# Kernel tuning notes

Hardware: AMD Instinct MI355X
Metric: run time of the kernel (lower is better)

Reference implementation:

```python
import jax, jax.numpy as jnp
import numpy as np

N, D_IN, D_H, N_HEADS, N_CLS = 8192, 384, 64, 4, 6
LN_EPS = 1e-5


def setup_inputs() -> dict:
    key = jax.random.key(0)
    ks = jax.random.split(key, 8)
    x = jax.random.normal(ks[0], (N, D_IN), dtype=jnp.float32)
    proj_w = jax.random.normal(ks[1], (D_IN, D_H), dtype=jnp.float32) / np.sqrt(D_IN)
    proj_b = jnp.zeros((D_H,), jnp.float32)
    head_w = jax.random.normal(ks[2], (N_HEADS, D_H, D_H), dtype=jnp.float32) / np.sqrt(D_H)
    head_b = jnp.zeros((N_HEADS, D_H), jnp.float32)
    attn_w = jnp.ones((N_HEADS,), jnp.float32)  # nn.Parameter(torch.ones(num_heads))
    gamma = jnp.ones((D_H,), jnp.float32)
    beta = jnp.zeros((D_H,), jnp.float32)
    fc_w = jax.random.normal(ks[3], (D_H, N_CLS), dtype=jnp.float32) / np.sqrt(D_H)
    fc_b = jnp.zeros((N_CLS,), jnp.float32)
    return {"x": x, "proj_w": proj_w, "proj_b": proj_b, "head_w": head_w,
            "head_b": head_b, "attn_w": attn_w, "gamma": gamma, "beta": beta,
            "fc_w": fc_w, "fc_b": fc_b}


def _safe_cdist_sq_to_dist(sq):
    # Euclidean distance with zero (sub)gradient at zero distance, matching torch.cdist.
    pos = sq > 0
    return jnp.where(pos, jnp.sqrt(jnp.where(pos, sq, 1.0)), 0.0)


def reference(x, proj_w, proj_b, head_w, head_b, attn_w, gamma, beta, fc_w, fc_b):
    h = jax.nn.relu(x @ proj_w + proj_b)                      # [N, D_H]
    hp = jnp.einsum('nd,hde->hne', h, head_w) + head_b[:, None, :]  # [H, N, D_H]
    sumsq = jnp.sum(hp * hp, axis=-1)                          # [H, N]
    sq = sumsq[:, :, None] + sumsq[:, None, :] - 2.0 * jnp.einsum('hnd,hmd->hnm', hp, hp)
    dist = _safe_cdist_sq_to_dist(jnp.maximum(sq, 0.0))        # [H, N, N]
    scores = jax.nn.softmax(-dist, axis=-1)                    # [H, N, N]
    h_head = jnp.einsum('hnm,hmd->hnd', scores, hp)            # [H, N, D_H]
    aw = jax.nn.softmax(attn_w, axis=0)                        # [H]
    combined = jnp.einsum('h,hnd->nd', aw, h_head)             # [N, D_H]
    mu = jnp.mean(combined, axis=-1, keepdims=True)
    var = jnp.mean((combined - mu) ** 2, axis=-1, keepdims=True)
    normed = (combined - mu) * jax.lax.rsqrt(var + LN_EPS) * gamma + beta
    return normed @ fc_w + fc_b                                # [N, N_CLS]
```

## Files before the change

### kernel.cpp

```cpp
#include <hip/hip_runtime.h>

#define N_TOK 8192
#define D_IN 384
#define D_H 64
#define NHEADS 4
#define NSPLIT 4
#define N_CLS 6
#define LN_EPS 1e-5f

typedef __attribute__((ext_vector_type(8))) short short8;
typedef __attribute__((ext_vector_type(4))) float f32x4;

#define L2E2 2.08136898100560774f

__device__ __forceinline__ unsigned short f2bf(float f) {
    unsigned int u = __float_as_uint(f);
    u += 0x7FFFu + ((u >> 16) & 1u);
    return (unsigned short)(u >> 16);
}
__device__ __forceinline__ float bf2f(unsigned short s) {
    return __uint_as_float(((unsigned int)s) << 16);
}

__device__ __forceinline__ int kperm(int k) {
    return (k & 32) + 2 * (k & 15) + ((k >> 4) & 1);
}

__device__ __forceinline__ void gload_lds16(const void* g, void* l) {
    __builtin_amdgcn_global_load_lds(
        (const __attribute__((address_space(1))) unsigned int*)g,
        (__attribute__((address_space(3))) unsigned int*)l, 16, 0, 0);
}

__global__ __launch_bounds__(512) void stage1_kernel(
    const float* __restrict__ x, const float* __restrict__ proj_w,
    const float* __restrict__ proj_b, const float* __restrict__ head_w,
    const float* __restrict__ head_b,
    unsigned short* __restrict__ hp, unsigned short* __restrict__ Vf,
    float* __restrict__ ssq2)
{
    const int lane = threadIdx.x & 63;
    const int wv   = threadIdx.x >> 6;
    const int rb0  = blockIdx.x * 32;

    __shared__ float h_sh[32][68];
    __shared__ __align__(16) unsigned short vt[NHEADS][4][64][8];

    {
        float acc[4];
        float b = proj_b[lane];
        #pragma unroll
        for (int r = 0; r < 4; ++r) acc[r] = b;
        const float* x0 = x + (size_t)(rb0 + wv * 4) * D_IN;
        #pragma unroll 2
        for (int k4 = 0; k4 < D_IN / 4; ++k4) {
            float w0 = proj_w[(k4 * 4 + 0) * 64 + lane];
            float w1 = proj_w[(k4 * 4 + 1) * 64 + lane];
            float w2 = proj_w[(k4 * 4 + 2) * 64 + lane];
            float w3 = proj_w[(k4 * 4 + 3) * 64 + lane];
            #pragma unroll
            for (int r = 0; r < 4; ++r) {
                float4 xv = *(const float4*)(x0 + r * D_IN + k4 * 4);
                acc[r] = fmaf(xv.x, w0, acc[r]);
                acc[r] = fmaf(xv.y, w1, acc[r]);
                acc[r] = fmaf(xv.z, w2, acc[r]);
                acc[r] = fmaf(xv.w, w3, acc[r]);
            }
        }
        #pragma unroll
        for (int r = 0; r < 4; ++r)
            h_sh[wv * 4 + r][lane] = fmaxf(acc[r], 0.f);
    }
    __syncthreads();

    const int head = wv >> 1;
    const int half = wv & 1;
    float a[16];
    {
        float b = head_b[head * 64 + lane];
        #pragma unroll
        for (int r = 0; r < 16; ++r) a[r] = b;
    }
    const float* wb = head_w + head * 64 * 64;
    #pragma unroll 2
    for (int e4 = 0; e4 < 16; ++e4) {
        float w0 = wb[(e4 * 4 + 0) * 64 + lane];
        float w1 = wb[(e4 * 4 + 1) * 64 + lane];
        float w2 = wb[(e4 * 4 + 2) * 64 + lane];
        float w3 = wb[(e4 * 4 + 3) * 64 + lane];
        #pragma unroll
        for (int r = 0; r < 16; ++r) {
            float4 hv = *(const float4*)&h_sh[half * 16 + r][e4 * 4];
            a[r] = fmaf(hv.x, w0, a[r]);
            a[r] = fmaf(hv.y, w1, a[r]);
            a[r] = fmaf(hv.z, w2, a[r]);
            a[r] = fmaf(hv.w, w3, a[r]);
        }
    }

    #pragma unroll
    for (int r = 0; r < 16; ++r) {
        int kl  = half * 16 + r;
        int row = rb0 + kl;
        unsigned short hb = f2bf(a[r]);
        float hf = bf2f(hb);
        hp[((size_t)head * N_TOK + row) * 64 + lane] = hb;
        int p = kperm(row & 63);
        vt[head][(p >> 3) & 3][lane][p & 7] = hb;
        float s = hf * hf;
        #pragma unroll
        for (int off = 32; off > 0; off >>= 1) s += __shfl_xor(s, off);
        if (lane == 0) ssq2[head * N_TOK + row] = s * L2E2;
    }
    __syncthreads();

    const int kgbase = (rb0 & 32) ? 4 : 0;
    #pragma unroll
    for (int i = 0; i < 2; ++i) {
        int c  = threadIdx.x + 512 * i;
        int hc = c >> 8, rem = c & 255;
        int kg = rem >> 6, d = rem & 63;
        short8 v = *(const short8*)&vt[hc][kg][d][0];
        *(short8*)&Vf[(((size_t)hc * (N_TOK / 8) + (rb0 >> 6) * 8 + kgbase + kg) * 64
                       + d) * 8] = v;
    }
}

__global__ __launch_bounds__(256, 4) void flash_kernel(
    const unsigned short* __restrict__ hp, const unsigned short* __restrict__ Vf,
    const float* __restrict__ ssq2, unsigned short* __restrict__ Og,
    float* __restrict__ Lg)
{
    const int head  = blockIdx.x & 3;
    const int split = blockIdx.x >> 2;
    const int q0    = blockIdx.y * 128;
    const int w     = threadIdx.x >> 6;
    const int lane  = threadIdx.x & 63;
    const int col   = lane & 15;
    const int quad  = lane >> 4;
    const int tid   = threadIdx.x;

    __shared__ __align__(16) unsigned short Psh[4][2][16][64];
    __shared__ __align__(16) unsigned short Kst[2][4096];
    __shared__ __align__(16) unsigned short Vst[2][4096];

    const unsigned short* hpH = hp + head * (N_TOK * 64);
    const unsigned short* VfH = Vf + head * (N_TOK * 64);
    const float* ssqH = ssq2 + head * N_TOK;

    const int rb = q0 + w * 32;
    const bool diag_lo = ((rb >> 5) & 1) == 0;

    short8 aQ[2][2];
    float ssqn2[2][4];
    #pragma unroll
    for (int s = 0; s < 2; ++s) {
        const unsigned short* qrow = hpH + (rb + s * 16 + col) * 64;
        aQ[s][0] = *(const short8*)(qrow + quad * 8);
        aQ[s][1] = *(const short8*)(qrow + 32 + quad * 8);
        #pragma unroll
        for (int r = 0; r < 4; ++r)
            ssqn2[s][r] = ssqH[rb + s * 16 + quad * 4 + r];
    }

    const f32x4 zero4 = {0.f, 0.f, 0.f, 0.f};
    f32x4 accO[2][4] = {{zero4, zero4, zero4, zero4}, {zero4, zero4, zero4, zero4}};
    f32x4 accL[2] = {zero4, zero4};
    const short8 ones = {16256,16256,16256,16256,16256,16256,16256,16256};
    const float NEG2L2 = -2.0f * L2E2;

    const int koff0 = (((tid & ~7) | ((tid & 7) ^ ((tid >> 3) & 7))) << 4);
    const int karow = col * 128 + ((quad ^ (col & 7)) << 4);
    const int va    = (quad * 64 + col) << 4;
    const int wcb   = quad * 512 + ((((col >> 2) ^ ((quad & 1) << 2)) << 4))
                      + ((col & 3) << 2);

    const int kt0   = split * 32;
    const int ktend = kt0 + 32;

    {
        const char* kg = (const char*)(hpH + kt0 * 4096);
        const char* vg = (const char*)(VfH + kt0 * 4096);
        gload_lds16(kg + koff0,        (char*)&Kst[0][0] + tid * 16);
        gload_lds16(kg + koff0 + 4096, (char*)&Kst[0][0] + tid * 16 + 4096);
        gload_lds16(vg + tid * 16,        (char*)&Vst[0][0] + tid * 16);
        gload_lds16(vg + tid * 16 + 4096, (char*)&Vst[0][0] + tid * 16 + 4096);
    }
    float smc[4];
    #pragma unroll
    for (int nt = 0; nt < 4; ++nt) smc[nt] = ssqH[kt0 * 64 + nt * 16 + col];
    __syncthreads();

    #pragma unroll 1
    for (int kt = kt0; kt < ktend; ++kt) {
        const int p = (kt - kt0) & 1;
        const char* Kb = (const char*)&Kst[p][0];
        const char* Vb = (const char*)&Vst[p][0];
        const bool has_next = (kt + 1 < ktend);

        float smn[4];
        if (has_next) {
            const char* kgn = (const char*)(hpH + (kt + 1) * 4096);
            const char* vgn = (const char*)(VfH + (kt + 1) * 4096);
            char* Kn = (char*)&Kst[p ^ 1][0];
            char* Vn = (char*)&Vst[p ^ 1][0];
            gload_lds16(kgn + koff0,        Kn + tid * 16);
            gload_lds16(kgn + koff0 + 4096, Kn + tid * 16 + 4096);
            gload_lds16(vgn + tid * 16,        Vn + tid * 16);
            gload_lds16(vgn + tid * 16 + 4096, Vn + tid * 16 + 4096);
            #pragma unroll
            for (int nt = 0; nt < 4; ++nt)
                smn[nt] = ssqH[(kt + 1) * 64 + nt * 16 + col];
        }

        f32x4 aSA[2][2] = {{zero4, zero4}, {zero4, zero4}};
        {
            short8 k0 = *(const short8*)(Kb + karow);
            short8 k1 = *(const short8*)(Kb + (karow ^ 64));
            short8 k2 = *(const short8*)(Kb + 2048 + karow);
            short8 k3 = *(const short8*)(Kb + 2048 + (karow ^ 64));
            aSA[0][0] = __builtin_amdgcn_mfma_f32_16x16x32_bf16(aQ[0][0], k0, aSA[0][0], 0, 0, 0);
            aSA[0][0] = __builtin_amdgcn_mfma_f32_16x16x32_bf16(aQ[0][1], k1, aSA[0][0], 0, 0, 0);
            aSA[1][0] = __builtin_amdgcn_mfma_f32_16x16x32_bf16(aQ[1][0], k0, aSA[1][0], 0, 0, 0);
            aSA[1][0] = __builtin_amdgcn_mfma_f32_16x16x32_bf16(aQ[1][1], k1, aSA[1][0], 0, 0, 0);
            aSA[0][1] = __builtin_amdgcn_mfma_f32_16x16x32_bf16(aQ[0][0], k2, aSA[0][1], 0, 0, 0);
            aSA[0][1] = __builtin_amdgcn_mfma_f32_16x16x32_bf16(aQ[0][1], k3, aSA[0][1], 0, 0, 0);
            aSA[1][1] = __builtin_amdgcn_mfma_f32_16x16x32_bf16(aQ[1][0], k2, aSA[1][1], 0, 0, 0);
            aSA[1][1] = __builtin_amdgcn_mfma_f32_16x16x32_bf16(aQ[1][1], k3, aSA[1][1], 0, 0, 0);
        }

        #pragma unroll
        for (int s = 0; s < 2; ++s) {
            char* pB = (char*)&Psh[w][s][0][0];
            float pf0[4], pf1[4];
            #pragma unroll
            for (int r = 0; r < 4; ++r) {
                float sq0 = fmaf(aSA[s][0][r], NEG2L2, ssqn2[s][r] + smc[0]);
                pf0[r] = __builtin_amdgcn_exp2f(-__builtin_amdgcn_sqrtf(fmaxf(sq0, 0.f)));
                float sq1 = fmaf(aSA[s][1][r], NEG2L2, ssqn2[s][r] + smc[1]);
                pf1[r] = __builtin_amdgcn_exp2f(-__builtin_amdgcn_sqrtf(fmaxf(sq1, 0.f)));
            }
            #pragma unroll
            for (int r = 0; r < 4; ++r) {
                unsigned int d0 = __builtin_amdgcn_perm(__float_as_uint(pf1[r]),
                                                        __float_as_uint(pf0[r]), 0x07060302u);
                *(unsigned int*)(pB + ((wcb ^ (r << 4)) + r * 128)) = d0;
            }
        }
        if (diag_lo && kt == (rb >> 6) && lane < 16) {
            #pragma unroll
            for (int s = 0; s < 2; ++s) {
                int t = ((rb + s * 16) >> 4) & 3;
                int sc2 = 4 * lane + 2 * (t & 1);
                int ad = lane * 128 + (((lane >> 2) ^ (lane & 7)) << 4) + (sc2 & 15);
                *(unsigned short*)((char*)&Psh[w][s][0][0] + ad) = 0x3F80;
            }
        }

        f32x4 aSB[2][2] = {{zero4, zero4}, {zero4, zero4}};
        {
            short8 k0 = *(const short8*)(Kb + 4096 + karow);
            short8 k1 = *(const short8*)(Kb + 4096 + (karow ^ 64));
            short8 k2 = *(const short8*)(Kb + 6144 + karow);
            short8 k3 = *(const short8*)(Kb + 6144 + (karow ^ 64));
            aSB[0][0] = __builtin_amdgcn_mfma_f32_16x16x32_bf16(aQ[0][0], k0, aSB[0][0], 0, 0, 0);
            aSB[0][0] = __builtin_amdgcn_mfma_f32_16x16x32_bf16(aQ[0][1], k1, aSB[0][0], 0, 0, 0);
            aSB[1][0] = __builtin_amdgcn_mfma_f32_16x16x32_bf16(aQ[1][0], k0, aSB[1][0], 0, 0, 0);
            aSB[1][0] = __builtin_amdgcn_mfma_f32_16x16x32_bf16(aQ[1][1], k1, aSB[1][0], 0, 0, 0);
            aSB[0][1] = __builtin_amdgcn_mfma_f32_16x16x32_bf16(aQ[0][0], k2, aSB[0][1], 0, 0, 0);
            aSB[0][1] = __builtin_amdgcn_mfma_f32_16x16x32_bf16(aQ[0][1], k3, aSB[0][1], 0, 0, 0);
            aSB[1][1] = __builtin_amdgcn_mfma_f32_16x16x32_bf16(aQ[1][0], k2, aSB[1][1], 0, 0, 0);
            aSB[1][1] = __builtin_amdgcn_mfma_f32_16x16x32_bf16(aQ[1][1], k3, aSB[1][1], 0, 0, 0);
        }

        #pragma unroll
        for (int s = 0; s < 2; ++s) {
            char* pB = (char*)&Psh[w][s][0][0];
            float pf2[4], pf3[4];
            #pragma unroll
            for (int r = 0; r < 4; ++r) {
                float sq2 = fmaf(aSB[s][0][r], NEG2L2, ssqn2[s][r] + smc[2]);
                pf2[r] = __builtin_amdgcn_exp2f(-__builtin_amdgcn_sqrtf(fmaxf(sq2, 0.f)));
                float sq3 = fmaf(aSB[s][1][r], NEG2L2, ssqn2[s][r] + smc[3]);
                pf3[r] = __builtin_amdgcn_exp2f(-__builtin_amdgcn_sqrtf(fmaxf(sq3, 0.f)));
            }
            #pragma unroll
            for (int r = 0; r < 4; ++r) {
                unsigned int d1 = __builtin_amdgcn_perm(__float_as_uint(pf3[r]),
                                                        __float_as_uint(pf2[r]), 0x07060302u);
                *(unsigned int*)(pB + (((wcb ^ (r << 4)) + r * 128) ^ 64)) = d1;
            }
        }
        if (!diag_lo && kt == (rb >> 6) && lane < 16) {
            #pragma unroll
            for (int s = 0; s < 2; ++s) {
                int t = ((rb + s * 16) >> 4) & 3;
                int sc2 = 4 * lane + 2 * (t & 1);
                int ad = (lane * 128 + (((lane >> 2) ^ (lane & 7)) << 4) + (sc2 & 15)) ^ 64;
                *(unsigned short*)((char*)&Psh[w][s][0][0] + ad) = 0x3F80;
            }
        }

        {
            const char* p0 = (const char*)&Psh[w][0][0][0];
            const char* p1 = (const char*)&Psh[w][1][0][0];
            short8 aP0 = *(const short8*)(p0 + karow);
            short8 aP1 = *(const short8*)(p1 + karow);
            short8 bV[4];
            #pragma unroll
            for (int dt = 0; dt < 4; ++dt)
                bV[dt] = *(const short8*)(Vb + va + dt * 256);
            accL[0] = __builtin_amdgcn_mfma_f32_16x16x32_bf16(aP0, ones, accL[0], 0, 0, 0);
            accL[1] = __builtin_amdgcn_mfma_f32_16x16x32_bf16(aP1, ones, accL[1], 0, 0, 0);
            #pragma unroll
            for (int dt = 0; dt < 4; ++dt) {
                accO[0][dt] = __builtin_amdgcn_mfma_f32_16x16x32_bf16(aP0, bV[dt], accO[0][dt], 0, 0, 0);
                accO[1][dt] = __builtin_amdgcn_mfma_f32_16x16x32_bf16(aP1, bV[dt], accO[1][dt], 0, 0, 0);
            }
            short8 aP0b = *(const short8*)(p0 + (karow ^ 64));
            short8 aP1b = *(const short8*)(p1 + (karow ^ 64));
            #pragma unroll
            for (int dt = 0; dt < 4; ++dt)
                bV[dt] = *(const short8*)(Vb + va + dt * 256 + 4096);
            accL[0] = __builtin_amdgcn_mfma_f32_16x16x32_bf16(aP0b, ones, accL[0], 0, 0, 0);
            accL[1] = __builtin_amdgcn_mfma_f32_16x16x32_bf16(aP1b, ones, accL[1], 0, 0, 0);
            #pragma unroll
            for (int dt = 0; dt < 4; ++dt) {
                accO[0][dt] = __builtin_amdgcn_mfma_f32_16x16x32_bf16(aP0b, bV[dt], accO[0][dt], 0, 0, 0);
                accO[1][dt] = __builtin_amdgcn_mfma_f32_16x16x32_bf16(aP1b, bV[dt], accO[1][dt], 0, 0, 0);
            }
        }

        __syncthreads();
        if (has_next) {
            smc[0] = smn[0]; smc[1] = smn[1]; smc[2] = smn[2]; smc[3] = smn[3];
        }
    }

    unsigned short* og = Og + (size_t)(split * NHEADS + head) * N_TOK * 64;
    float* lg = Lg + (size_t)(split * NHEADS + head) * N_TOK;
    #pragma unroll
    for (int s = 0; s < 2; ++s)
        #pragma unroll
        for (int r = 0; r < 4; ++r) {
            int row = rb + s * 16 + quad * 4 + r;
            #pragma unroll
            for (int dt = 0; dt < 4; ++dt)
                og[row * 64 + dt * 16 + col] = f2bf(accO[s][dt][r]);
            if (col == 0) lg[row] = accL[s][r];
        }
}

__global__ __launch_bounds__(256) void combine_kernel(
    const unsigned short* __restrict__ Og, const float* __restrict__ Lg,
    const float* __restrict__ attn_w, const float* __restrict__ gamma,
    const float* __restrict__ beta, const float* __restrict__ fc_w,
    const float* __restrict__ fc_b, float* __restrict__ out)
{
    const int lane = threadIdx.x & 63;
    const int ty   = threadIdx.x >> 6;
    const int row  = blockIdx.x * 4 + ty;

    float a0 = attn_w[0], a1 = attn_w[1], a2 = attn_w[2], a3 = attn_w[3];
    float m = fmaxf(fmaxf(a0, a1), fmaxf(a2, a3));
    float e0 = __expf(a0 - m), e1 = __expf(a1 - m), e2 = __expf(a2 - m), e3 = __expf(a3 - m);
    float inv = 1.f / (e0 + e1 + e2 + e3);
    float aw[4] = {e0 * inv, e1 * inv, e2 * inv, e3 * inv};

    float c = 0.f;
    #pragma unroll
    for (int hh = 0; hh < NHEADS; ++hh) {
        float l = 0.f, o = 0.f;
        #pragma unroll
        for (int s = 0; s < NSPLIT; ++s) {
            l += Lg[(s * NHEADS + hh) * N_TOK + row];
            o += bf2f(Og[(size_t)((s * NHEADS + hh) * N_TOK + row) * 64 + lane]);
        }
        c += aw[hh] * o * __builtin_amdgcn_rcpf(l);
    }

    float s = c;
    #pragma unroll
    for (int off = 32; off > 0; off >>= 1) s += __shfl_xor(s, off);
    float mu = s * (1.f / 64.f);
    float d = c - mu;
    float v = d * d;
    #pragma unroll
    for (int off = 32; off > 0; off >>= 1) v += __shfl_xor(v, off);
    float normed = d * rsqrtf(v * (1.f / 64.f) + LN_EPS) * gamma[lane] + beta[lane];

    float lg[N_CLS];
    #pragma unroll
    for (int cc = 0; cc < N_CLS; ++cc) {
        float p = normed * fc_w[lane * N_CLS + cc];
        #pragma unroll
        for (int off = 32; off > 0; off >>= 1) p += __shfl_xor(p, off);
        lg[cc] = p;
    }
    if (lane == 0) {
        #pragma unroll
        for (int cc = 0; cc < N_CLS; ++cc)
            out[row * N_CLS + cc] = lg[cc] + fc_b[cc];
    }
}

extern "C" void kernel_launch(void* const* d_in, const int* in_sizes, int n_in,
                              void* d_out, int out_size, void* d_ws, size_t ws_size,
                              hipStream_t stream)
{
    const float* x      = (const float*)d_in[0];
    const float* proj_w = (const float*)d_in[1];
    const float* proj_b = (const float*)d_in[2];
    const float* head_w = (const float*)d_in[3];
    const float* head_b = (const float*)d_in[4];
    const float* attn_w = (const float*)d_in[5];
    const float* gamma  = (const float*)d_in[6];
    const float* beta   = (const float*)d_in[7];
    const float* fc_w   = (const float*)d_in[8];
    const float* fc_b   = (const float*)d_in[9];
    float* out = (float*)d_out;

    char* ws = (char*)d_ws;
    unsigned short* hp = (unsigned short*)(ws);
    unsigned short* Vf = (unsigned short*)(ws + (4u << 20));
    float* ssq2 = (float*)(ws + (8u << 20));
    unsigned short* Og = (unsigned short*)(ws + (8u << 20) + (128u << 10));
    float* Lg   = (float*)(ws + (24u << 20) + (128u << 10));

    stage1_kernel<<<N_TOK / 32, 512, 0, stream>>>(x, proj_w, proj_b, head_w, head_b,
                                                  hp, Vf, ssq2);
    dim3 g2(NHEADS * NSPLIT, N_TOK / 128);
    flash_kernel<<<g2, 256, 0, stream>>>(hp, Vf, ssq2, Og, Lg);
    combine_kernel<<<N_TOK / 4, 256, 0, stream>>>(Og, Lg, attn_w, gamma, beta,
                                                  fc_w, fc_b, out);
}
```

Baseline: 234.0 us.

## Process query sub-tiles sequentially per warp with single P staging buffer

Restructures the inner flash loop so each warp handles its two 16-row query sub-tiles one after another. Each pass runs the full QK^T, the exp/sqrt scoring and the PV accumulation before moving on, instead of splitting the key tile into two halves across both sub-tiles. This halves the per-warp P staging buffer in shared memory and simplifies the diagonal fixup. In exchange, K and V fragments are reloaded from LDS once per sub-tile, and there is less independent MFMA work in flight to hide latency.

Result: slower. 419.0 us (+79.1%).

```diff
diff --git a/kernel.cpp b/kernel.cpp
--- a/kernel.cpp
+++ b/kernel.cpp
@@ -140,7 +140,7 @@
     const int quad  = lane >> 4;
     const int tid   = threadIdx.x;
 
-    __shared__ __align__(16) unsigned short Psh[4][2][16][64];
+    __shared__ __align__(16) unsigned short Psh[4][16][64];
     __shared__ __align__(16) unsigned short Kst[2][4096];
     __shared__ __align__(16) unsigned short Vst[2][4096];
 
@@ -149,7 +149,6 @@
     const float* ssqH = ssq2 + head * N_TOK;
 
     const int rb = q0 + w * 32;
-    const bool diag_lo = ((rb >> 5) & 1) == 0;
 
     short8 aQ[2][2];
     float ssqn2[2][4];
@@ -213,121 +212,78 @@
                 smn[nt] = ssqH[(kt + 1) * 64 + nt * 16 + col];
         }
 
-        f32x4 aSA[2][2] = {{zero4, zero4}, {zero4, zero4}};
-        {
-            short8 k0 = *(const short8*)(Kb + karow);
-            short8 k1 = *(const short8*)(Kb + (karow ^ 64));
-            short8 k2 = *(const short8*)(Kb + 2048 + karow);
-            short8 k3 = *(const short8*)(Kb + 2048 + (karow ^ 64));
-            aSA[0][0] = __builtin_amdgcn_mfma_f32_16x16x32_bf16(aQ[0][0], k0, aSA[0][0], 0, 0, 0);
-            aSA[0][0] = __builtin_amdgcn_mfma_f32_16x16x32_bf16(aQ[0][1], k1, aSA[0][0], 0, 0, 0);
-            aSA[1][0] = __builtin_amdgcn_mfma_f32_16x16x32_bf16(aQ[1][0], k0, aSA[1][0], 0, 0, 0);
-            aSA[1][0] = __builtin_amdgcn_mfma_f32_16x16x32_bf16(aQ[1][1], k1, aSA[1][0], 0, 0, 0);
-            aSA[0][1] = __builtin_amdgcn_mfma_f32_16x16x32_bf16(aQ[0][0], k2, aSA[0][1], 0, 0, 0);
-            aSA[0][1] = __builtin_amdgcn_mfma_f32_16x16x32_bf16(aQ[0][1], k3, aSA[0][1], 0, 0, 0);
-            aSA[1][1] = __builtin_amdgcn_mfma_f32_16x16x32_bf16(aQ[1][0], k2, aSA[1][1], 0, 0, 0);
-            aSA[1][1] = __builtin_amdgcn_mfma_f32_16x16x32_bf16(aQ[1][1], k3, aSA[1][1], 0, 0, 0);
-        }
+        char* pB = (char*)&Psh[w][0][0];
 
         #pragma unroll
         for (int s = 0; s < 2; ++s) {
-            char* pB = (char*)&Psh[w][s][0][0];
-            float pf0[4], pf1[4];
-            #pragma unroll
-            for (int r = 0; r < 4; ++r) {
-                float sq0 = fmaf(aSA[s][0][r], NEG2L2, ssqn2[s][r] + smc[0]);
-                pf0[r] = __builtin_amdgcn_exp2f(-__builtin_amdgcn_sqrtf(fmaxf(sq0, 0.f)));
-                float sq1 = fmaf(aSA[s][1][r], NEG2L2, ssqn2[s][r] + smc[1]);
-                pf1[r] = __builtin_amdgcn_exp2f(-__builtin_amdgcn_sqrtf(fmaxf(sq1, 0.f)));
-            }
-            #pragma unroll
-            for (int r = 0; r < 4; ++r) {
-                unsigned int d0 = __builtin_amdgcn_perm(__float_as_uint(pf1[r]),
-                                                        __float_as_uint(pf0[r]), 0x07060302u);
-                *(unsigned int*)(pB + ((wcb ^ (r << 4)) + r * 128)) = d0;
-            }
-        }
-        if (diag_lo && kt == (rb >> 6) && lane < 16) {
-            #pragma unroll
-            for (int s = 0; s < 2; ++s) {
+            f32x4 aS[4] = {zero4, zero4, zero4, zero4};
+            {
+                short8 k0 = *(const short8*)(Kb + karow);
+                short8 k1 = *(const short8*)(Kb + (karow ^ 64));
+                short8 k2 = *(const short8*)(Kb + 2048 + karow);
+                short8 k3 = *(const short8*)(Kb + 2048 + (karow ^ 64));
+                aS[0] = __builtin_amdgcn_mfma_f32_16x16x32_bf16(aQ[s][0], k0, aS[0], 0, 0, 0);
+                aS[0] = __builtin_amdgcn_mfma_f32_16x16x32_bf16(aQ[s][1], k1, aS[0], 0, 0, 0);
+                aS[1] = __builtin_amdgcn_mfma_f32_16x16x32_bf16(aQ[s][0], k2, aS[1], 0, 0, 0);
+                aS[1] = __builtin_amdgcn_mfma_f32_16x16x32_bf16(aQ[s][1], k3, aS[1], 0, 0, 0);
+                k0 = *(const short8*)(Kb + 4096 + karow);
+                k1 = *(const short8*)(Kb + 4096 + (karow ^ 64));
+                k2 = *(const short8*)(Kb + 6144 + karow);
+                k3 = *(const short8*)(Kb + 6144 + (karow ^ 64));
+                aS[2] = __builtin_amdgcn_mfma_f32_16x16x32_bf16(aQ[s][0], k0, aS[2], 0, 0, 0);
+                aS[2] = __builtin_amdgcn_mfma_f32_16x16x32_bf16(aQ[s][1], k1, aS[2], 0, 0, 0);
+                aS[3] = __builtin_amdgcn_mfma_f32_16x16x32_bf16(aQ[s][0], k2, aS[3], 0, 0, 0);
+                aS[3] = __builtin_amdgcn_mfma_f32_16x16x32_bf16(aQ[s][1], k3, aS[3], 0, 0, 0);
+            }
+
+            {
+                float pf[4][4];
+                #pragma unroll
+                for (int nt = 0; nt < 4; ++nt)
+                    #pragma unroll
+                    for (int r = 0; r < 4; ++r) {
+                        float sq = fmaf(aS[nt][r], NEG2L2, ssqn2[s][r] + smc[nt]);
+                        pf[nt][r] = __builtin_amdgcn_exp2f(
+                            -__builtin_amdgcn_sqrtf(fmaxf(sq, 0.f)));
+                    }
+                #pragma unroll
+                for (int r = 0; r < 4; ++r) {
+                    int ad = (wcb ^ (r << 4)) + r * 128;
+                    unsigned int d0 = __builtin_amdgcn_perm(__float_as_uint(pf[1][r]),
+                                                            __float_as_uint(pf[0][r]), 0x07060302u);
+                    *(unsigned int*)(pB + ad) = d0;
+                    unsigned int d1 = __builtin_amdgcn_perm(__float_as_uint(pf[3][r]),
+                                                            __float_as_uint(pf[2][r]), 0x07060302u);
+                    *(unsigned int*)(pB + (ad ^ 64)) = d1;
+                }
+            }
+            if (kt == (rb >> 6) && lane < 16) {
                 int t = ((rb + s * 16) >> 4) & 3;
-                int sc2 = 4 * lane + 2 * (t & 1);
-                int ad = lane * 128 + (((lane >> 2) ^ (lane & 7)) << 4) + (sc2 & 15);
-                *(unsigned short*)((char*)&Psh[w][s][0][0] + ad) = 0x3F80;
-            }
-        }
-
-        f32x4 aSB[2][2] = {{zero4, zero4}, {zero4, zero4}};
-        {
-            short8 k0 = *(const short8*)(Kb + 4096 + karow);
-            short8 k1 = *(const short8*)(Kb + 4096 + (karow ^ 64));
-            short8 k2 = *(const short8*)(Kb + 6144 + karow);
-            short8 k3 = *(const short8*)(Kb + 6144 + (karow ^ 64));
-            aSB[0][0] = __builtin_amdgcn_mfma_f32_16x16x32_bf16(aQ[0][0], k0, aSB[0][0], 0, 0, 0);
-            aSB[0][0] = __builtin_amdgcn_mfma_f32_16x16x32_bf16(aQ[0][1], k1, aSB[0][0], 0, 0, 0);
-            aSB[1][0] = __builtin_amdgcn_mfma_f32_16x16x32_bf16(aQ[1][0], k0, aSB[1][0], 0, 0, 0);
-            aSB[1][0] = __builtin_amdgcn_mfma_f32_16x16x32_bf16(aQ[1][1], k1, aSB[1][0], 0, 0, 0);
-            aSB[0][1] = __builtin_amdgcn_mfma_f32_16x16x32_bf16(aQ[0][0], k2, aSB[0][1], 0, 0, 0);
-            aSB[0][1] = __builtin_amdgcn_mfma_f32_16x16x32_bf16(aQ[0][1], k3, aSB[0][1], 0, 0, 0);
-            aSB[1][1] = __builtin_amdgcn_mfma_f32_16x16x32_bf16(aQ[1][0], k2, aSB[1][1], 0, 0, 0);
-            aSB[1][1] = __builtin_amdgcn_mfma_f32_16x16x32_bf16(aQ[1][1], k3, aSB[1][1], 0, 0, 0);
-        }
-
-        #pragma unroll
-        for (int s = 0; s < 2; ++s) {
-            char* pB = (char*)&Psh[w][s][0][0];
-            float pf2[4], pf3[4];
-            #pragma unroll
-            for (int r = 0; r < 4; ++r) {
-                float sq2 = fmaf(aSB[s][0][r], NEG2L2, ssqn2[s][r] + smc[2]);
-                pf2[r] = __builtin_amdgcn_exp2f(-__builtin_amdgcn_sqrtf(fmaxf(sq2, 0.f)));
-                float sq3 = fmaf(aSB[s][1][r], NEG2L2, ssqn2[s][r] + smc[3]);
-                pf3[r] = __builtin_amdgcn_exp2f(-__builtin_amdgcn_sqrtf(fmaxf(sq3, 0.f)));
-            }
-            #pragma unroll
-            for (int r = 0; r < 4; ++r) {
-                unsigned int d1 = __builtin_amdgcn_perm(__float_as_uint(pf3[r]),
-                                                        __float_as_uint(pf2[r]), 0x07060302u);
-                *(unsigned int*)(pB + (((wcb ^ (r << 4)) + r * 128) ^ 64)) = d1;
-            }
-        }
-        if (!diag_lo && kt == (rb >> 6) && lane < 16) {
-            #pragma unroll
-            for (int s = 0; s < 2; ++s) {
-                int t = ((rb + s * 16) >> 4) & 3;
-                int sc2 = 4 * lane + 2 * (t & 1);
-                int ad = (lane * 128 + (((lane >> 2) ^ (lane & 7)) << 4) + (sc2 & 15)) ^ 64;
-                *(unsigned short*)((char*)&Psh[w][s][0][0] + ad) = 0x3F80;
-            }
-        }
-
-        {
-            const char* p0 = (const char*)&Psh[w][0][0][0];
-            const char* p1 = (const char*)&Psh[w][1][0][0];
-            short8 aP0 = *(const short8*)(p0 + karow);
-            short8 aP1 = *(const short8*)(p1 + karow);
-            short8 bV[4];
-            #pragma unroll
-            for (int dt = 0; dt < 4; ++dt)
-                bV[dt] = *(const short8*)(Vb + va + dt * 256);
-            accL[0] = __builtin_amdgcn_mfma_f32_16x16x32_bf16(aP0, ones, accL[0], 0, 0, 0);
-            accL[1] = __builtin_amdgcn_mfma_f32_16x16x32_bf16(aP1, ones, accL[1], 0, 0, 0);
-            #pragma unroll
-            for (int dt = 0; dt < 4; ++dt) {
-                accO[0][dt] = __builtin_amdgcn_mfma_f32_16x16x32_bf16(aP0, bV[dt], accO[0][dt], 0, 0, 0);
-                accO[1][dt] = __builtin_amdgcn_mfma_f32_16x16x32_bf16(aP1, bV[dt], accO[1][dt], 0, 0, 0);
-            }
-            short8 aP0b = *(const short8*)(p0 + (karow ^ 64));
-            short8 aP1b = *(const short8*)(p1 + (karow ^ 64));
-            #pragma unroll
-            for (int dt = 0; dt < 4; ++dt)
-                bV[dt] = *(const short8*)(Vb + va + dt * 256 + 4096);
-            accL[0] = __builtin_amdgcn_mfma_f32_16x16x32_bf16(aP0b, ones, accL[0], 0, 0, 0);
-            accL[1] = __builtin_amdgcn_mfma_f32_16x16x32_bf16(aP1b, ones, accL[1], 0, 0, 0);
-            #pragma unroll
-            for (int dt = 0; dt < 4; ++dt) {
-                accO[0][dt] = __builtin_amdgcn_mfma_f32_16x16x32_bf16(aP0b, bV[dt], accO[0][dt], 0, 0, 0);
-                accO[1][dt] = __builtin_amdgcn_mfma_f32_16x16x32_bf16(aP1b, bV[dt], accO[1][dt], 0, 0, 0);
+                int ad = lane * 128 + (((lane >> 2) ^ (lane & 7)) << 4)
+                         + ((4 * lane + 2 * (t & 1)) & 15);
+                if (t & 2) ad ^= 64;
+                *(unsigned short*)(pB + ad) = 0x3F80;
+            }
+
+            {
+                short8 aP = *(const short8*)(pB + karow);
+                short8 bV[4];
+                #pragma unroll
+                for (int dt = 0; dt < 4; ++dt)
+                    bV[dt] = *(const short8*)(Vb + va + dt * 256);
+                accL[s] = __builtin_amdgcn_mfma_f32_16x16x32_bf16(aP, ones, accL[s], 0, 0, 0);
+                #pragma unroll
+                for (int dt = 0; dt < 4; ++dt)
+                    accO[s][dt] = __builtin_amdgcn_mfma_f32_16x16x32_bf16(aP, bV[dt], accO[s][dt], 0, 0, 0);
+
+                short8 aPb = *(const short8*)(pB + (karow ^ 64));
+                #pragma unroll
+                for (int dt = 0; dt < 4; ++dt)
+                    bV[dt] = *(const short8*)(Vb + va + dt * 256 + 4096);
+                accL[s] = __builtin_amdgcn_mfma_f32_16x16x32_bf16(aPb, ones, accL[s], 0, 0, 0);
+                #pragma unroll
+                for (int dt = 0; dt < 4; ++dt)
+                    accO[s][dt] = __builtin_amdgcn_mfma_f32_16x16x32_bf16(aPb, bV[dt], accO[s][dt], 0, 0, 0);
             }
         }
 
```
